# Performance work log

Hardware: AMD Instinct MI355X
Metric: run time of the kernel (lower is better)

## Reference

```python
import jax, jax.numpy as jnp
import numpy as np

N_NODES = 20000
N_EDGES = 160000
IN_F = 128
HID_HEADS, HID_CH = 32, 32
OUT_EMB = 64
NEG_SLOPE = 0.2


def setup_inputs() -> dict:
    key = jax.random.key(0)
    ks = jax.random.split(key, 8)
    x = jax.random.normal(ks[0], (N_NODES, IN_F), dtype=jnp.float32)
    edge_index = jax.random.randint(ks[1], (2, N_EDGES), 0, N_NODES, dtype=jnp.int32)
    W1 = jax.random.normal(ks[2], (IN_F, HID_HEADS * HID_CH), dtype=jnp.float32) / np.sqrt(IN_F)
    att_src1 = jax.random.normal(ks[3], (HID_HEADS, HID_CH), dtype=jnp.float32) / np.sqrt(HID_CH)
    att_dst1 = jax.random.normal(ks[4], (HID_HEADS, HID_CH), dtype=jnp.float32) / np.sqrt(HID_CH)
    b1 = jnp.zeros((HID_HEADS * HID_CH,), dtype=jnp.float32)
    W2 = jax.random.normal(ks[5], (HID_HEADS * HID_CH, OUT_EMB), dtype=jnp.float32) / np.sqrt(HID_HEADS * HID_CH)
    att_src2 = jax.random.normal(ks[6], (1, OUT_EMB), dtype=jnp.float32) / np.sqrt(OUT_EMB)
    att_dst2 = jax.random.normal(ks[7], (1, OUT_EMB), dtype=jnp.float32) / np.sqrt(OUT_EMB)
    b2 = jnp.zeros((OUT_EMB,), dtype=jnp.float32)
    return {"x": x, "edge_index": edge_index, "W1": W1, "att_src1": att_src1,
            "att_dst1": att_dst1, "b1": b1, "W2": W2, "att_src2": att_src2,
            "att_dst2": att_dst2, "b2": b2}


def _gat_conv(x, src, dst, W, a_src, a_dst, b, n_nodes):
    # PyG GATConv (eval mode): per-head linear, edge attention, segment softmax over
    # incoming edges of each target node, weighted scatter-sum, concat heads + bias.
    H, C = a_src.shape
    h = (x @ W).reshape(-1, H, C)                       # [N, H, C]
    e_s = jnp.einsum('nhc,hc->nh', h, a_src)            # [N, H]
    e_d = jnp.einsum('nhc,hc->nh', h, a_dst)            # [N, H]
    e = jax.nn.leaky_relu(e_s[src] + e_d[dst], NEG_SLOPE)  # [E, H]
    m = jax.ops.segment_max(e, dst, num_segments=n_nodes)  # [N, H]
    m = jnp.where(jnp.isfinite(m), m, jnp.zeros_like(m))   # nodes w/o in-edges
    ex = jnp.exp(e - m[dst])                            # [E, H]
    s = jax.ops.segment_sum(ex, dst, num_segments=n_nodes)
    alpha = ex / (s[dst] + 1e-16)                       # [E, H]
    msg = h[src] * alpha[:, :, None]                    # [E, H, C]
    out = jax.ops.segment_sum(msg, dst, num_segments=n_nodes)  # [N, H, C]
    return out.reshape(n_nodes, H * C) + b


def reference(x, edge_index, W1, att_src1, att_dst1, b1, W2, att_src2, att_dst2, b2):
    n = x.shape[0]
    loops = jnp.arange(n, dtype=edge_index.dtype)
    src = jnp.concatenate([edge_index[0], loops])  # PyG adds self-loops by default
    dst = jnp.concatenate([edge_index[1], loops])
    h = jax.nn.elu(_gat_conv(x, src, dst, W1, att_src1, att_dst1, b1, n))
    out = _gat_conv(h, src, dst, W2, att_src2, att_dst2, b2, n)
    return out
```

## Files before the change

kernel.cpp:

```cpp
#include <hip/hip_runtime.h>
#include <hip/hip_bf16.h>
#include <math.h>

typedef __attribute__((ext_vector_type(8))) short bf16x8;
typedef __attribute__((ext_vector_type(4))) float f32x4;
typedef __attribute__((ext_vector_type(8))) unsigned short u16x8;

__device__ inline float bf2f(unsigned short u) {
    union { float f; unsigned int i; } c; c.i = ((unsigned int)u) << 16; return c.f;
}
__device__ inline unsigned short f2bf(float f) {
    union { float f; unsigned int i; } c; c.f = f;
    unsigned int r = c.i + 0x7fffu + ((c.i >> 16) & 1u);
    return (unsigned short)(r >> 16);
}

__global__ void cast_f32_bf16(const float* __restrict__ in, unsigned short* __restrict__ out,
                              int count4) {
    int i = blockIdx.x * blockDim.x + threadIdx.x;
    if (i >= count4) return;
    float4 v = *(const float4*)&in[(size_t)i * 4];
    ushort4 o;
    o.x = f2bf(v.x); o.y = f2bf(v.y); o.z = f2bf(v.z); o.w = f2bf(v.w);
    *(ushort4*)&out[(size_t)i * 4] = o;
}

__global__ void transpose_cast(const float* __restrict__ W, unsigned short* __restrict__ WT,
                               int K, int N) {
    int idx = blockIdx.x * blockDim.x + threadIdx.x;
    if (idx >= K * N) return;
    int nn = idx / K, kk = idx - nn * K;
    WT[idx] = f2bf(W[(size_t)kk * N + nn]);
}

__global__ __launch_bounds__(256) void gemm_mfma_attn(const unsigned short* __restrict__ A,
                                                      const unsigned short* __restrict__ BT,
                                                      unsigned short* __restrict__ C,
                                                      const float* __restrict__ asrc,
                                                      const float* __restrict__ adst,
                                                      float* __restrict__ es,
                                                      float* __restrict__ ed,
                                                      int M, int N, int K) {
    int tid = threadIdx.x;
    int wid = tid >> 6, lane = tid & 63;
    int wm = wid >> 1, wn = wid & 1;
    int m0 = blockIdx.x * 64 + wm * 32;
    int n0 = blockIdx.y * 64 + wn * 32;
    int lr = lane & 15;
    int q  = lane >> 4;
    int lk = q * 8;

    int ra0 = min(m0 + lr, M - 1);
    int ra1 = min(m0 + 16 + lr, M - 1);
    const unsigned short* pa0 = A + (size_t)ra0 * K + lk;
    const unsigned short* pa1 = A + (size_t)ra1 * K + lk;
    const unsigned short* pb0 = BT + (size_t)(n0 + lr) * K + lk;
    const unsigned short* pb1 = BT + (size_t)(n0 + 16 + lr) * K + lk;

    f32x4 acc00 = {0,0,0,0}, acc01 = {0,0,0,0}, acc10 = {0,0,0,0}, acc11 = {0,0,0,0};
    for (int k = 0; k < K; k += 64) {
        bf16x8 a0 = *(const bf16x8*)(pa0 + k);
        bf16x8 a1 = *(const bf16x8*)(pa1 + k);
        bf16x8 b0 = *(const bf16x8*)(pb0 + k);
        bf16x8 b1 = *(const bf16x8*)(pb1 + k);
        bf16x8 a0b = *(const bf16x8*)(pa0 + k + 32);
        bf16x8 a1b = *(const bf16x8*)(pa1 + k + 32);
        bf16x8 b0b = *(const bf16x8*)(pb0 + k + 32);
        bf16x8 b1b = *(const bf16x8*)(pb1 + k + 32);
        acc00 = __builtin_amdgcn_mfma_f32_16x16x32_bf16(a0, b0, acc00, 0, 0, 0);
        acc01 = __builtin_amdgcn_mfma_f32_16x16x32_bf16(a0, b1, acc01, 0, 0, 0);
        acc10 = __builtin_amdgcn_mfma_f32_16x16x32_bf16(a1, b0, acc10, 0, 0, 0);
        acc11 = __builtin_amdgcn_mfma_f32_16x16x32_bf16(a1, b1, acc11, 0, 0, 0);
        acc00 = __builtin_amdgcn_mfma_f32_16x16x32_bf16(a0b, b0b, acc00, 0, 0, 0);
        acc01 = __builtin_amdgcn_mfma_f32_16x16x32_bf16(a0b, b1b, acc01, 0, 0, 0);
        acc10 = __builtin_amdgcn_mfma_f32_16x16x32_bf16(a1b, b0b, acc10, 0, 0, 0);
        acc11 = __builtin_amdgcn_mfma_f32_16x16x32_bf16(a1b, b1b, acc11, 0, 0, 0);
    }
    int srow = q * 4;
    #pragma unroll
    for (int r = 0; r < 4; ++r) {
        int r0 = m0 + srow + r, r1 = m0 + 16 + srow + r;
        if (r0 < M) {
            C[(size_t)r0 * N + n0 + lr]      = f2bf(acc00[r]);
            C[(size_t)r0 * N + n0 + 16 + lr] = f2bf(acc01[r]);
        }
        if (r1 < M) {
            C[(size_t)r1 * N + n0 + lr]      = f2bf(acc10[r]);
            C[(size_t)r1 * N + n0 + 16 + lr] = f2bf(acc11[r]);
        }
    }
    int head = blockIdx.y * 2 + wn;
    float as_lo = asrc[head * 32 + lr], as_hi = asrc[head * 32 + 16 + lr];
    float ad_lo = adst[head * 32 + lr], ad_hi = adst[head * 32 + 16 + lr];
    #pragma unroll
    for (int X = 0; X < 2; ++X) {
        f32x4 ac0 = X ? acc10 : acc00;
        f32x4 ac1 = X ? acc11 : acc01;
        #pragma unroll
        for (int r = 0; r < 4; ++r) {
            float ps = ac0[r] * as_lo + ac1[r] * as_hi;
            float pd = ac0[r] * ad_lo + ac1[r] * ad_hi;
            #pragma unroll
            for (int msk = 1; msk < 16; msk <<= 1) {
                ps += __shfl_xor(ps, msk);
                pd += __shfl_xor(pd, msk);
            }
            int row = m0 + X * 16 + q * 4 + r;
            if (lr == 0 && row < M) {
                es[row * 32 + head] = ps;
                ed[row * 32 + head] = pd;
            }
        }
    }
}

__global__ __launch_bounds__(256) void gemm2_fused(const unsigned short* __restrict__ A,
                                                   const unsigned short* __restrict__ BT,
                                                   unsigned short* __restrict__ C,
                                                   const float* __restrict__ asrc,
                                                   const float* __restrict__ adst,
                                                   float* __restrict__ es,
                                                   float* __restrict__ ed, int M) {
    const int K = 1024;
    int tid = threadIdx.x, wid = tid >> 6, lane = tid & 63;
    int m0 = blockIdx.x * 32;
    int lr = lane & 15, q = lane >> 4, lk = q * 8;
    int k0 = wid * 256;

    const unsigned short* pa0 = A + (size_t)(m0 + lr) * K + k0 + lk;
    const unsigned short* pa1 = A + (size_t)(m0 + 16 + lr) * K + k0 + lk;
    const unsigned short* pb0 = BT + (size_t)(0  + lr) * K + k0 + lk;
    const unsigned short* pb1 = BT + (size_t)(16 + lr) * K + k0 + lk;
    const unsigned short* pb2 = BT + (size_t)(32 + lr) * K + k0 + lk;
    const unsigned short* pb3 = BT + (size_t)(48 + lr) * K + k0 + lk;

    f32x4 acc[2][4] = {};
    for (int k = 0; k < 256; k += 64) {
        bf16x8 a0  = *(const bf16x8*)(pa0 + k);
        bf16x8 a1  = *(const bf16x8*)(pa1 + k);
        bf16x8 a0b = *(const bf16x8*)(pa0 + k + 32);
        bf16x8 a1b = *(const bf16x8*)(pa1 + k + 32);
        bf16x8 b0  = *(const bf16x8*)(pb0 + k);
        bf16x8 b0b = *(const bf16x8*)(pb0 + k + 32);
        acc[0][0] = __builtin_amdgcn_mfma_f32_16x16x32_bf16(a0,  b0,  acc[0][0], 0, 0, 0);
        acc[1][0] = __builtin_amdgcn_mfma_f32_16x16x32_bf16(a1,  b0,  acc[1][0], 0, 0, 0);
        acc[0][0] = __builtin_amdgcn_mfma_f32_16x16x32_bf16(a0b, b0b, acc[0][0], 0, 0, 0);
        acc[1][0] = __builtin_amdgcn_mfma_f32_16x16x32_bf16(a1b, b0b, acc[1][0], 0, 0, 0);
        bf16x8 b1  = *(const bf16x8*)(pb1 + k);
        bf16x8 b1b = *(const bf16x8*)(pb1 + k + 32);
        acc[0][1] = __builtin_amdgcn_mfma_f32_16x16x32_bf16(a0,  b1,  acc[0][1], 0, 0, 0);
        acc[1][1] = __builtin_amdgcn_mfma_f32_16x16x32_bf16(a1,  b1,  acc[1][1], 0, 0, 0);
        acc[0][1] = __builtin_amdgcn_mfma_f32_16x16x32_bf16(a0b, b1b, acc[0][1], 0, 0, 0);
        acc[1][1] = __builtin_amdgcn_mfma_f32_16x16x32_bf16(a1b, b1b, acc[1][1], 0, 0, 0);
        bf16x8 b2  = *(const bf16x8*)(pb2 + k);
        bf16x8 b2b = *(const bf16x8*)(pb2 + k + 32);
        acc[0][2] = __builtin_amdgcn_mfma_f32_16x16x32_bf16(a0,  b2,  acc[0][2], 0, 0, 0);
        acc[1][2] = __builtin_amdgcn_mfma_f32_16x16x32_bf16(a1,  b2,  acc[1][2], 0, 0, 0);
        acc[0][2] = __builtin_amdgcn_mfma_f32_16x16x32_bf16(a0b, b2b, acc[0][2], 0, 0, 0);
        acc[1][2] = __builtin_amdgcn_mfma_f32_16x16x32_bf16(a1b, b2b, acc[1][2], 0, 0, 0);
        bf16x8 b3  = *(const bf16x8*)(pb3 + k);
        bf16x8 b3b = *(const bf16x8*)(pb3 + k + 32);
        acc[0][3] = __builtin_amdgcn_mfma_f32_16x16x32_bf16(a0,  b3,  acc[0][3], 0, 0, 0);
        acc[1][3] = __builtin_amdgcn_mfma_f32_16x16x32_bf16(a1,  b3,  acc[1][3], 0, 0, 0);
        acc[0][3] = __builtin_amdgcn_mfma_f32_16x16x32_bf16(a0b, b3b, acc[0][3], 0, 0, 0);
        acc[1][3] = __builtin_amdgcn_mfma_f32_16x16x32_bf16(a1b, b3b, acc[1][3], 0, 0, 0);
    }
    __shared__ float red[4][32][64];
    #pragma unroll
    for (int rf = 0; rf < 2; ++rf)
        #pragma unroll
        for (int cf = 0; cf < 4; ++cf)
            #pragma unroll
            for (int i = 0; i < 4; ++i)
                red[wid][rf * 16 + q * 4 + i][cf * 16 + lr] = acc[rf][cf][i];
    __syncthreads();
    int r = tid >> 3, c0 = (tid & 7) * 8;
    float v[8];
    #pragma unroll
    for (int j = 0; j < 8; ++j)
        v[j] = red[0][r][c0 + j] + red[1][r][c0 + j] + red[2][r][c0 + j] + red[3][r][c0 + j];
    u16x8 o8;
    float ps = 0.f, pd = 0.f;
    #pragma unroll
    for (int j = 0; j < 8; ++j) {
        o8[j] = f2bf(v[j]);
        ps += v[j] * asrc[c0 + j];
        pd += v[j] * adst[c0 + j];
    }
    int row = m0 + r;
    *(u16x8*)&C[(size_t)row * 64 + c0] = o8;
    #pragma unroll
    for (int msk = 1; msk < 8; msk <<= 1) {
        ps += __shfl_xor(ps, msk);
        pd += __shfl_xor(pd, msk);
    }
    if ((tid & 7) == 0) { es[row] = ps; ed[row] = pd; }
}

__global__ void count_edges(const int* __restrict__ ei, int* __restrict__ counts,
                            int E0, int n) {
    int e = blockIdx.x * blockDim.x + threadIdx.x;
    int Etot = E0 + n;
    if (e >= Etot) return;
    int dst = (e < E0) ? ei[E0 + e] : (e - E0);
    atomicAdd(&counts[dst], 1);
}

__global__ void scan_excl(const int* __restrict__ counts, int* __restrict__ offsets, int n) {
    __shared__ int wpre[16];
    __shared__ int total_s;
    __shared__ int running_s;
    int tid = threadIdx.x, lane = tid & 63, w = tid >> 6;
    if (tid == 0) running_s = 0;
    __syncthreads();
    for (int base = 0; base < n; base += 1024) {
        int i = base + tid;
        int v = (i < n) ? counts[i] : 0;
        int incl = v;
        #pragma unroll
        for (int d = 1; d < 64; d <<= 1) {
            int t = __shfl_up(incl, d);
            if (lane >= d) incl += t;
        }
        if (lane == 63) wpre[w] = incl;
        __syncthreads();
        if (w == 0) {
            int s = (lane < 16) ? wpre[lane] : 0;
            int sc = s;
            #pragma unroll
            for (int d = 1; d < 16; d <<= 1) {
                int t = __shfl_up(sc, d);
                if (lane >= d) sc += t;
            }
            if (lane < 16) wpre[lane] = sc - s;
            if (lane == 15) total_s = sc;
        }
        __syncthreads();
        int r = running_s;
        if (i < n) offsets[i] = r + wpre[w] + incl - v;
        __syncthreads();
        if (tid == 0) running_s = r + total_s;
        __syncthreads();
    }
    if (tid == 0) offsets[n] = running_s;
}

__global__ void fill_edges(const int* __restrict__ ei, const int* __restrict__ offsets,
                           int* __restrict__ cursor, int* __restrict__ srcs,
                           int E0, int n) {
    int e = blockIdx.x * blockDim.x + threadIdx.x;
    int Etot = E0 + n;
    if (e >= Etot) return;
    int src, dst;
    if (e < E0) { src = ei[e]; dst = ei[E0 + e]; }
    else        { src = dst = e - E0; }
    int pos = offsets[dst] + atomicAdd(&cursor[dst], 1);
    srcs[pos] = src;
}

__global__ __launch_bounds__(256) void gat1_agg(const unsigned short* __restrict__ hb,
                                                const float* __restrict__ es,
                                                const float* __restrict__ ed,
                                                const int* __restrict__ offsets,
                                                const int* __restrict__ srcs,
                                                const float* __restrict__ b1,
                                                unsigned short* __restrict__ out, int n) {
    int node = blockIdx.x;
    int tid = threadIdx.x;
    int h2 = tid & 31, j2 = tid >> 5;
    int ep = tid >> 7, t2 = tid & 127;
    int head = t2 >> 2, c8 = (t2 & 3) * 8;
    int hoff = head * 32 + c8;

    __shared__ unsigned short lds_et[128][32];
    __shared__ float sed[32];
    __shared__ float red[4][32];
    __shared__ float sinv_s[32];
    __shared__ float lcomb[128][9];

    int beg = offsets[node], end = offsets[node + 1];
    if (tid < 32) sed[tid] = ed[node * 32 + tid];
    __syncthreads();
    float edh = sed[h2];
    float ssum = 0.f;
    float a[8] = {0.f,0.f,0.f,0.f,0.f,0.f,0.f,0.f};

    for (int c0 = beg; c0 < end; c0 += 128) {
        int lim = min(128, end - c0);
        for (int eloc = j2; eloc < lim; eloc += 8) {
            int s = srcs[c0 + eloc];
            float ev = es[s * 32 + h2] + edh;
            ev = ev > 0.f ? ev : 0.2f * ev;
            unsigned short w16 = f2bf(__expf(ev));
            lds_et[eloc][h2] = w16;
            ssum += bf2f(w16);
        }
        __syncthreads();
        int eloc = ep;
        for (; eloc + 2 < lim; eloc += 4) {
            int s0 = srcs[c0 + eloc], s1 = srcs[c0 + eloc + 2];
            float t0 = bf2f(lds_et[eloc][head]);
            float t1 = bf2f(lds_et[eloc + 2][head]);
            u16x8 h0 = *(const u16x8*)&hb[(size_t)s0 * 1024 + hoff];
            u16x8 h1 = *(const u16x8*)&hb[(size_t)s1 * 1024 + hoff];
            #pragma unroll
            for (int j = 0; j < 8; ++j) a[j] += t0 * bf2f(h0[j]) + t1 * bf2f(h1[j]);
        }
        if (eloc < lim) {
            int s0 = srcs[c0 + eloc];
            float t0 = bf2f(lds_et[eloc][head]);
            u16x8 h0 = *(const u16x8*)&hb[(size_t)s0 * 1024 + hoff];
            #pragma unroll
            for (int j = 0; j < 8; ++j) a[j] += t0 * bf2f(h0[j]);
        }
        __syncthreads();
    }

    ssum += __shfl_xor(ssum, 32);
    int w = tid >> 6;
    if ((tid & 63) < 32) red[w][h2] = ssum;
    if (ep == 1) {
        #pragma unroll
        for (int j = 0; j < 8; ++j) lcomb[t2][j] = a[j];
    }
    __syncthreads();
    if (tid < 32) {
        float s = red[0][tid] + red[1][tid] + red[2][tid] + red[3][tid];
        sinv_s[tid] = 1.0f / (s + 1e-16f);
    }
    __syncthreads();
    if (ep == 0) {
        float si = sinv_s[head];
        float4 bl = *(const float4*)&b1[hoff];
        float4 bh = *(const float4*)&b1[hoff + 4];
        float bb[8] = {bl.x, bl.y, bl.z, bl.w, bh.x, bh.y, bh.z, bh.w};
        u16x8 o8;
        #pragma unroll
        for (int j = 0; j < 8; ++j) {
            float r = (a[j] + lcomb[t2][j]) * si + bb[j];
            r = r > 0.f ? r : expm1f(r);
            o8[j] = f2bf(r);
        }
        *(u16x8*)&out[(size_t)node * 1024 + hoff] = o8;
    }
}

__global__ void stats2(const float* __restrict__ es, const float* __restrict__ ed,
                       const int* __restrict__ offsets, const int* __restrict__ srcs,
                       float* __restrict__ et2, float* __restrict__ sinv2, int n) {
    int node = blockIdx.x * (blockDim.x >> 6) + (threadIdx.x >> 6);
    int lane = threadIdx.x & 63;
    if (node >= n) return;
    int beg = offsets[node], end = offsets[node + 1];
    float edv = ed[node];
    float ssum = 0.f;
    for (int e = beg + lane; e < end; e += 64) {
        float ev = es[srcs[e]] + edv;
        ev = ev > 0.f ? ev : 0.2f * ev;
        float t = __expf(ev);
        et2[e] = t;
        ssum += t;
    }
    #pragma unroll
    for (int o = 1; o < 64; o <<= 1) ssum += __shfl_xor(ssum, o);
    if (lane == 0) sinv2[node] = 1.0f / (ssum + 1e-16f);
}

__global__ void gather2(const unsigned short* __restrict__ hb2,
                        const float* __restrict__ et2,
                        const float* __restrict__ sinv2,
                        const int* __restrict__ offsets, const int* __restrict__ srcs,
                        const float* __restrict__ b2, float* __restrict__ out, int n) {
    int node = blockIdx.x * (blockDim.x >> 6) + (threadIdx.x >> 6);
    int lane = threadIdx.x & 63;
    if (node >= n) return;
    int beg = offsets[node], end = offsets[node + 1];
    float acc = 0.f;
    int e = beg;
    for (; e + 3 < end; e += 4) {
        int s0 = srcs[e], s1 = srcs[e + 1], s2 = srcs[e + 2], s3 = srcs[e + 3];
        float t0 = et2[e], t1 = et2[e + 1], t2 = et2[e + 2], t3 = et2[e + 3];
        acc += t0 * bf2f(hb2[(size_t)s0 * 64 + lane])
             + t1 * bf2f(hb2[(size_t)s1 * 64 + lane])
             + t2 * bf2f(hb2[(size_t)s2 * 64 + lane])
             + t3 * bf2f(hb2[(size_t)s3 * 64 + lane]);
    }
    for (; e < end; ++e) {
        acc += et2[e] * bf2f(hb2[(size_t)srcs[e] * 64 + lane]);
    }
    out[(size_t)node * 64 + lane] = acc * sinv2[node] + b2[lane];
}

extern "C" void kernel_launch(void* const* d_in, const int* in_sizes, int n_in,
                              void* d_out, int out_size, void* d_ws, size_t ws_size,
                              hipStream_t stream) {
    const float* x        = (const float*)d_in[0];
    const int*   ei       = (const int*)d_in[1];
    const float* W1       = (const float*)d_in[2];
    const float* att_src1 = (const float*)d_in[3];
    const float* att_dst1 = (const float*)d_in[4];
    const float* b1       = (const float*)d_in[5];
    const float* W2       = (const float*)d_in[6];
    const float* att_src2 = (const float*)d_in[7];
    const float* att_dst2 = (const float*)d_in[8];
    const float* b2       = (const float*)d_in[9];
    float* out = (float*)d_out;

    int n  = in_sizes[0] / 128;
    int E0 = in_sizes[1] / 2;
    int Etot = E0 + n;

    float* ws = (float*)d_ws;
    size_t off = 0;
    unsigned short* hb1 = (unsigned short*)(ws + off); off += (size_t)n * 512;
    unsigned short* hact = (unsigned short*)(ws + off); off += (size_t)n * 512;
    unsigned short* hb2 = (unsigned short*)(ws + off); off += (size_t)n * 32;
    unsigned short* xb  = (unsigned short*)(ws + off); off += (size_t)n * 64;
    unsigned short* W1T = (unsigned short*)(ws + off); off += 1024 * 128 / 2;
    unsigned short* W2T = (unsigned short*)(ws + off); off += 64 * 1024 / 2;
    float* es1  = ws + off; off += (size_t)n * 32;
    float* ed1  = ws + off; off += (size_t)n * 32;
    float* et2  = ws + off; off += (size_t)Etot;
    float* sinv2 = ws + off; off += (size_t)n;
    int* counts  = (int*)(ws + off); off += n;
    int* cursor  = (int*)(ws + off); off += n;
    int* offsets = (int*)(ws + off); off += n + 8;
    int* srcs    = (int*)(ws + off); off += Etot;
    float* es2 = es1;
    float* ed2 = ed1;

    cast_f32_bf16<<<(n * 128 / 4 + 255) / 256, 256, 0, stream>>>(x, xb, n * 128 / 4);
    transpose_cast<<<(128 * 1024 + 255) / 256, 256, 0, stream>>>(W1, W1T, 128, 1024);
    transpose_cast<<<(1024 * 64 + 255) / 256, 256, 0, stream>>>(W2, W2T, 1024, 64);

    hipMemsetAsync(counts, 0, 2 * (size_t)n * sizeof(int), stream);
    count_edges<<<(Etot + 255) / 256, 256, 0, stream>>>(ei, counts, E0, n);
    scan_excl<<<1, 1024, 0, stream>>>(counts, offsets, n);
    fill_edges<<<(Etot + 255) / 256, 256, 0, stream>>>(ei, offsets, cursor, srcs, E0, n);

    gemm_mfma_attn<<<dim3((n + 63) / 64, 1024 / 64), 256, 0, stream>>>(
        xb, W1T, hb1, att_src1, att_dst1, es1, ed1, n, 1024, 128);
    gat1_agg<<<n, 256, 0, stream>>>(hb1, es1, ed1, offsets, srcs, b1, hact, n);

    gemm2_fused<<<n / 32, 256, 0, stream>>>(hact, W2T, hb2, att_src2, att_dst2, es2, ed2, n);
    stats2<<<(n + 3) / 4, 256, 0, stream>>>(es2, ed2, offsets, srcs, et2, sinv2, n);
    gather2<<<(n + 3) / 4, 256, 0, stream>>>(hb2, et2, sinv2, offsets, srcs, b2, out, n);
}
```

Baseline: 203.0 us.

## Fuse layer-2 softmax and gather, stage GEMM output via LDS, merge weight prep

```diff
diff --git a/kernel.cpp b/kernel.cpp
--- a/kernel.cpp
+++ b/kernel.cpp
@@ -25,12 +25,19 @@
     *(ushort4*)&out[(size_t)i * 4] = o;
 }
 
-__global__ void transpose_cast(const float* __restrict__ W, unsigned short* __restrict__ WT,
-                               int K, int N) {
+__global__ void prep_weights(const float* __restrict__ W1, unsigned short* __restrict__ W1T,
+                             const float* __restrict__ W2, unsigned short* __restrict__ W2T) {
     int idx = blockIdx.x * blockDim.x + threadIdx.x;
-    if (idx >= K * N) return;
-    int nn = idx / K, kk = idx - nn * K;
-    WT[idx] = f2bf(W[(size_t)kk * N + nn]);
+    const int n1 = 128 * 1024;
+    const int n2 = 1024 * 64;
+    if (idx < n1) {
+        int nn = idx / 128, kk = idx - nn * 128;
+        W1T[idx] = f2bf(W1[(size_t)kk * 1024 + nn]);
+    } else if (idx < n1 + n2) {
+        int i2 = idx - n1;
+        int nn = i2 / 1024, kk = i2 - nn * 1024;
+        W2T[i2] = f2bf(W2[(size_t)kk * 64 + nn]);
+    }
 }
 
 __global__ __launch_bounds__(256) void gemm_mfma_attn(const unsigned short* __restrict__ A,
@@ -44,8 +51,9 @@
     int tid = threadIdx.x;
     int wid = tid >> 6, lane = tid & 63;
     int wm = wid >> 1, wn = wid & 1;
-    int m0 = blockIdx.x * 64 + wm * 32;
-    int n0 = blockIdx.y * 64 + wn * 32;
+    int m0b = blockIdx.x * 64, n0b = blockIdx.y * 64;
+    int m0 = m0b + wm * 32;
+    int n0 = n0b + wn * 32;
     int lr = lane & 15;
     int q  = lane >> 4;
     int lk = q * 8;
@@ -76,17 +84,25 @@
         acc10 = __builtin_amdgcn_mfma_f32_16x16x32_bf16(a1b, b0b, acc10, 0, 0, 0);
         acc11 = __builtin_amdgcn_mfma_f32_16x16x32_bf16(a1b, b1b, acc11, 0, 0, 0);
     }
+    __shared__ unsigned short ct[64][68];
     int srow = q * 4;
     #pragma unroll
     for (int r = 0; r < 4; ++r) {
-        int r0 = m0 + srow + r, r1 = m0 + 16 + srow + r;
-        if (r0 < M) {
-            C[(size_t)r0 * N + n0 + lr]      = f2bf(acc00[r]);
-            C[(size_t)r0 * N + n0 + 16 + lr] = f2bf(acc01[r]);
-        }
-        if (r1 < M) {
-            C[(size_t)r1 * N + n0 + lr]      = f2bf(acc10[r]);
-            C[(size_t)r1 * N + n0 + 16 + lr] = f2bf(acc11[r]);
+        ct[wm * 32 + srow + r][wn * 32 + lr]          = f2bf(acc00[r]);
+        ct[wm * 32 + srow + r][wn * 32 + 16 + lr]     = f2bf(acc01[r]);
+        ct[wm * 32 + 16 + srow + r][wn * 32 + lr]     = f2bf(acc10[r]);
+        ct[wm * 32 + 16 + srow + r][wn * 32 + 16 + lr] = f2bf(acc11[r]);
+    }
+    __syncthreads();
+    {
+        int row = tid >> 2, cs = (tid & 3) * 16;
+        int gr = m0b + row;
+        if (gr < M) {
+            u16x8 v0, v1;
+            #pragma unroll
+            for (int j = 0; j < 8; ++j) { v0[j] = ct[row][cs + j]; v1[j] = ct[row][cs + 8 + j]; }
+            *(u16x8*)&C[(size_t)gr * N + n0b + cs]     = v0;
+            *(u16x8*)&C[(size_t)gr * N + n0b + cs + 8] = v1;
         }
     }
     int head = blockIdx.y * 2 + wn;
@@ -345,50 +361,49 @@
     }
 }
 
-__global__ void stats2(const float* __restrict__ es, const float* __restrict__ ed,
-                       const int* __restrict__ offsets, const int* __restrict__ srcs,
-                       float* __restrict__ et2, float* __restrict__ sinv2, int n) {
-    int node = blockIdx.x * (blockDim.x >> 6) + (threadIdx.x >> 6);
+__global__ __launch_bounds__(256) void gat2_agg(const unsigned short* __restrict__ hb2,
+                                                const float* __restrict__ es,
+                                                const float* __restrict__ ed,
+                                                const int* __restrict__ offsets,
+                                                const int* __restrict__ srcs,
+                                                const float* __restrict__ b2,
+                                                float* __restrict__ out, int n) {
+    int w = threadIdx.x >> 6;
+    int node = blockIdx.x * 4 + w;
     int lane = threadIdx.x & 63;
+    __shared__ float lt[4][64];
     if (node >= n) return;
     int beg = offsets[node], end = offsets[node + 1];
     float edv = ed[node];
-    float ssum = 0.f;
-    for (int e = beg + lane; e < end; e += 64) {
-        float ev = es[srcs[e]] + edv;
-        ev = ev > 0.f ? ev : 0.2f * ev;
-        float t = __expf(ev);
-        et2[e] = t;
+    float ssum = 0.f, acc = 0.f;
+    for (int c0 = beg; c0 < end; c0 += 64) {
+        int lim = min(64, end - c0);
+        float t = 0.f;
+        if (lane < lim) {
+            int s = srcs[c0 + lane];
+            float ev = es[s] + edv;
+            ev = ev > 0.f ? ev : 0.2f * ev;
+            t = __expf(ev);
+        }
+        lt[w][lane] = t;
         ssum += t;
+        asm volatile("s_waitcnt lgkmcnt(0)" ::: "memory");
+        int jj = 0;
+        for (; jj + 3 < lim; jj += 4) {
+            int s0 = srcs[c0 + jj], s1 = srcs[c0 + jj + 1];
+            int s2 = srcs[c0 + jj + 2], s3 = srcs[c0 + jj + 3];
+            acc += lt[w][jj]     * bf2f(hb2[(size_t)s0 * 64 + lane])
+                 + lt[w][jj + 1] * bf2f(hb2[(size_t)s1 * 64 + lane])
+                 + lt[w][jj + 2] * bf2f(hb2[(size_t)s2 * 64 + lane])
+                 + lt[w][jj + 3] * bf2f(hb2[(size_t)s3 * 64 + lane]);
+        }
+        for (; jj < lim; ++jj) {
+            acc += lt[w][jj] * bf2f(hb2[(size_t)srcs[c0 + jj] * 64 + lane]);
+        }
     }
     #pragma unroll
     for (int o = 1; o < 64; o <<= 1) ssum += __shfl_xor(ssum, o);
-    if (lane == 0) sinv2[node] = 1.0f / (ssum + 1e-16f);
-}
-
-__global__ void gather2(const unsigned short* __restrict__ hb2,
-                        const float* __restrict__ et2,
-                        const float* __restrict__ sinv2,
-                        const int* __restrict__ offsets, const int* __restrict__ srcs,
-                        const float* __restrict__ b2, float* __restrict__ out, int n) {
-    int node = blockIdx.x * (blockDim.x >> 6) + (threadIdx.x >> 6);
-    int lane = threadIdx.x & 63;
-    if (node >= n) return;
-    int beg = offsets[node], end = offsets[node + 1];
-    float acc = 0.f;
-    int e = beg;
-    for (; e + 3 < end; e += 4) {
-        int s0 = srcs[e], s1 = srcs[e + 1], s2 = srcs[e + 2], s3 = srcs[e + 3];
-        float t0 = et2[e], t1 = et2[e + 1], t2 = et2[e + 2], t3 = et2[e + 3];
-        acc += t0 * bf2f(hb2[(size_t)s0 * 64 + lane])
-             + t1 * bf2f(hb2[(size_t)s1 * 64 + lane])
-             + t2 * bf2f(hb2[(size_t)s2 * 64 + lane])
-             + t3 * bf2f(hb2[(size_t)s3 * 64 + lane]);
-    }
-    for (; e < end; ++e) {
-        acc += et2[e] * bf2f(hb2[(size_t)srcs[e] * 64 + lane]);
-    }
-    out[(size_t)node * 64 + lane] = acc * sinv2[node] + b2[lane];
+    out[(size_t)node * 64 + lane] = acc * (1.0f / (ssum + 1e-16f)) + b2[lane];
 }
 
 extern "C" void kernel_launch(void* const* d_in, const int* in_sizes, int n_in,
@@ -420,8 +435,6 @@
     unsigned short* W2T = (unsigned short*)(ws + off); off += 64 * 1024 / 2;
     float* es1  = ws + off; off += (size_t)n * 32;
     float* ed1  = ws + off; off += (size_t)n * 32;
-    float* et2  = ws + off; off += (size_t)Etot;
-    float* sinv2 = ws + off; off += (size_t)n;
     int* counts  = (int*)(ws + off); off += n;
     int* cursor  = (int*)(ws + off); off += n;
     int* offsets = (int*)(ws + off); off += n + 8;
@@ -430,8 +443,7 @@
     float* ed2 = ed1;
 
     cast_f32_bf16<<<(n * 128 / 4 + 255) / 256, 256, 0, stream>>>(x, xb, n * 128 / 4);
-    transpose_cast<<<(128 * 1024 + 255) / 256, 256, 0, stream>>>(W1, W1T, 128, 1024);
-    transpose_cast<<<(1024 * 64 + 255) / 256, 256, 0, stream>>>(W2, W2T, 1024, 64);
+    prep_weights<<<(128 * 1024 + 1024 * 64 + 255) / 256, 256, 0, stream>>>(W1, W1T, W2, W2T);
 
     hipMemsetAsync(counts, 0, 2 * (size_t)n * sizeof(int), stream);
     count_edges<<<(Etot + 255) / 256, 256, 0, stream>>>(ei, counts, E0, n);
@@ -443,6 +455,5 @@
     gat1_agg<<<n, 256, 0, stream>>>(hb1, es1, ed1, offsets, srcs, b1, hact, n);
 
     gemm2_fused<<<n / 32, 256, 0, stream>>>(hact, W2T, hb2, att_src2, att_dst2, es2, ed2, n);
-    stats2<<<(n + 3) / 4, 256, 0, stream>>>(es2, ed2, offsets, srcs, et2, sinv2, n);
-    gather2<<<(n + 3) / 4, 256, 0, stream>>>(hb2, et2, sinv2, offsets, srcs, b2, out, n);
-}
+    gat2_agg<<<(n + 3) / 4, 256, 0, stream>>>(hb2, es2, ed2, offsets, srcs, b2, out, n);
+}
```

Result: faster. 197.3 us (-2.8%).
